# Kernel optimization log

Hardware: AMD Instinct MI355X
Metric: run time of the kernel (lower is better)

Reference implementation:

```python
import jax, jax.numpy as jnp
import numpy as np

T, B, H, D = 128, 8, 8, 64


def setup_inputs() -> dict:
    key = jax.random.key(0)
    kA, kB, kS = jax.random.split(key, 3)
    # Gated-delta transition matrices: near-identity contractions so the
    # length-T matrix-product recurrence is numerically stable, mimicking
    # A_t = gamma_t * (I - beta_t k_t k_t^T) of the gated delta rule.
    eye = jnp.eye(D, dtype=jnp.float32)
    A = 0.9 * eye + 0.06 * jax.random.normal(kA, (T, B, H, D, D), dtype=jnp.float32)
    Bm = jax.random.normal(kB, (T, B, H, D, D), dtype=jnp.float32)
    init_state = jax.random.normal(kS, (B, H, D, D), dtype=jnp.float32)
    return {"A": A, "Bm": Bm, "init_state": init_state}


def reference(A, Bm, init_state):
    """Gated delta rule recurrence S_t = S_{t-1} @ A_t + B_t for all t,
    computed with a parallel associative scan (Blelloch-equivalent).

    A:  [T,B,H,D,D] transition matrices
    Bm: [T,B,H,D,D] additive updates
    init_state: [B,H,D,D]
    returns states: [T,B,H,D,D]
    """
    def combine(e1, e2):
        # apply e1 first, then e2:
        # (S A1 + B1) A2 + B2 = S (A1 A2) + (B1 A2 + B2)
        A1, B1 = e1
        A2, B2 = e2
        A12 = jnp.einsum('tbhij,tbhjk->tbhik', A1, A2)
        B12 = jnp.einsum('tbhij,tbhjk->tbhik', B1, A2) + B2
        return (A12, B12)

    cumA, cumB = jax.lax.associative_scan(combine, (A, Bm), axis=0)
    # S_t = init_state @ cumA_t + cumB_t
    states = jnp.einsum('bhij,tbhjk->tbhik', init_state, cumA) + cumB
    return states
```

## Files before the change

### kernel.cpp

```cpp
#include <hip/hip_runtime.h>


constexpr int kT = 128;
constexpr int kBH = 64;
constexpr int kD = 64;
constexpr int kNC = 8;
constexpr int kCH = kT / kNC;
constexpr int kP = 68;
constexpr int kTile = kD * kD;

typedef __attribute__((ext_vector_type(8))) short short8;
typedef __attribute__((ext_vector_type(4))) short short4v;
typedef __attribute__((ext_vector_type(4))) float f32x4;

__device__ __forceinline__ unsigned short f2bf(float f) {
  unsigned int u = __float_as_uint(f);
  u += 0x7FFFu + ((u >> 16) & 1u);
  return (unsigned short)(u >> 16);
}
__device__ __forceinline__ float bf2f(unsigned short h) {
  return __uint_as_float(((unsigned int)h) << 16);
}
__device__ __forceinline__ int swzi(int r, int c) { return (r * 64 + c) ^ ((r & 7) << 3); }

__device__ __forceinline__ const float* tile_ptr(const float* base, int t, int bh) {
  return base + ((size_t)(t * kBH + bh)) * kTile;
}

__device__ __forceinline__ f32x4 mfma16(short8 a, short8 b, f32x4 c) {
  return __builtin_amdgcn_mfma_f32_16x16x32_bf16(a, b, c, 0, 0, 0);
}

__device__ __forceinline__ void split4(const f32x4 v, short4v& h, short4v& l) {
#pragma unroll
  for (int i = 0; i < 4; ++i) {
    const unsigned short hh = f2bf(v[i]);
    h[i] = (short)hh;
    l[i] = (short)f2bf(v[i] - bf2f(hh));
  }
}

__global__ __launch_bounds__(256, 2) void gdr_k1(
    const float* __restrict__ A, const float* __restrict__ Bm,
    float* __restrict__ PA, float* __restrict__ PB) {
  __shared__ unsigned short sAh[4096], sAl[4096];
  __shared__ unsigned short sPAh[4096], sPAl[4096];
  __shared__ unsigned short sPBh[4096], sPBl[4096];

  const int tid = threadIdx.x;
  const int lane = tid & 63, wave = tid >> 6;
  const int wr = wave >> 1, wc = wave & 1;
  const int q = lane >> 4, l15 = lane & 15;
  const int bh = blockIdx.x >> 3, ck = blockIdx.x & 7;
  const int t0 = ck * kCH;
  const int an = lane;
  const int akb = wave;

  f32x4 apa[2][2], apb[2][2];
  {
    const float* At = tile_ptr(A, t0, bh);
    const float* Bt = tile_ptr(Bm, t0, bh);
#pragma unroll
    for (int mi = 0; mi < 2; ++mi)
#pragma unroll
      for (int ni = 0; ni < 2; ++ni) {
        const int off = (wc * 32 + ni * 16 + l15) * 64 + wr * 32 + mi * 16 + q * 4;
        apa[mi][ni] = *reinterpret_cast<const f32x4*>(At + off);
        apb[mi][ni] = *reinterpret_cast<const f32x4*>(Bt + off);
      }
  }

  float pfA[16];
  f32x4 pfB[2][2];
  {
    const float* At = tile_ptr(A, t0 + 1, bh);
    const float* Bt = tile_ptr(Bm, t0 + 1, bh);
#pragma unroll
    for (int kk = 0; kk < 16; ++kk) pfA[kk] = At[(akb * 16 + kk) * 64 + an];
#pragma unroll
    for (int mi = 0; mi < 2; ++mi)
#pragma unroll
      for (int ni = 0; ni < 2; ++ni)
        pfB[mi][ni] = *reinterpret_cast<const f32x4*>(
            Bt + (wc * 32 + ni * 16 + l15) * 64 + wr * 32 + mi * 16 + q * 4);
  }

  for (int t = t0 + 1; t < t0 + kCH; ++t) {
    if (t > t0 + 1) __syncthreads();
#pragma unroll
    for (int mi = 0; mi < 2; ++mi)
#pragma unroll
      for (int ni = 0; ni < 2; ++ni) {
        const int b = wc * 32 + ni * 16 + l15;
        const int a0 = wr * 32 + mi * 16 + q * 4;
        const int idx = swzi(b, a0);
        short4v h, l;
        split4(apa[mi][ni], h, l);
        *reinterpret_cast<short4v*>(&sPAh[idx]) = h;
        *reinterpret_cast<short4v*>(&sPAl[idx]) = l;
        split4(apb[mi][ni], h, l);
        *reinterpret_cast<short4v*>(&sPBh[idx]) = h;
        *reinterpret_cast<short4v*>(&sPBl[idx]) = l;
      }
#pragma unroll
    for (int s = 0; s < 2; ++s) {
      short8 h, l;
#pragma unroll
      for (int j = 0; j < 8; ++j) {
        const float v = pfA[s * 8 + j];
        const unsigned short hh = f2bf(v);
        h[j] = (short)hh;
        l[j] = (short)f2bf(v - bf2f(hh));
      }
      const int idx = swzi(an, akb * 16 + s * 8);
      *reinterpret_cast<short8*>(&sAh[idx]) = h;
      *reinterpret_cast<short8*>(&sAl[idx]) = l;
    }
    __syncthreads();

#pragma unroll
    for (int mi = 0; mi < 2; ++mi)
#pragma unroll
      for (int ni = 0; ni < 2; ++ni) {
        apa[mi][ni] = (f32x4){0.f, 0.f, 0.f, 0.f};
        apb[mi][ni] = pfB[mi][ni];
      }

    const int tn = (t + 1 < t0 + kCH) ? t + 1 : t;
    {
      const float* At = tile_ptr(A, tn, bh);
      const float* Bt = tile_ptr(Bm, tn, bh);
#pragma unroll
      for (int kk = 0; kk < 16; ++kk) pfA[kk] = At[(akb * 16 + kk) * 64 + an];
#pragma unroll
      for (int mi = 0; mi < 2; ++mi)
#pragma unroll
        for (int ni = 0; ni < 2; ++ni)
          pfB[mi][ni] = *reinterpret_cast<const f32x4*>(
              Bt + (wc * 32 + ni * 16 + l15) * 64 + wr * 32 + mi * 16 + q * 4);
    }

#pragma unroll
    for (int ks = 0; ks < 2; ++ks) {
      short8 xh[2], xl[2], yah[2], yal[2], ybh[2], ybl[2];
      const int colb = ks * 32 + q * 8;
#pragma unroll
      for (int mi = 0; mi < 2; ++mi) {
        const int idx = swzi(wr * 32 + mi * 16 + l15, colb);
        xh[mi] = *reinterpret_cast<const short8*>(&sAh[idx]);
        xl[mi] = *reinterpret_cast<const short8*>(&sAl[idx]);
      }
#pragma unroll
      for (int ni = 0; ni < 2; ++ni) {
        const int idx = swzi(wc * 32 + ni * 16 + l15, colb);
        yah[ni] = *reinterpret_cast<const short8*>(&sPAh[idx]);
        yal[ni] = *reinterpret_cast<const short8*>(&sPAl[idx]);
        ybh[ni] = *reinterpret_cast<const short8*>(&sPBh[idx]);
        ybl[ni] = *reinterpret_cast<const short8*>(&sPBl[idx]);
      }
#pragma unroll
      for (int mi = 0; mi < 2; ++mi)
#pragma unroll
        for (int ni = 0; ni < 2; ++ni) {
          apa[mi][ni] = mfma16(xh[mi], yah[ni], apa[mi][ni]);
          apa[mi][ni] = mfma16(xh[mi], yal[ni], apa[mi][ni]);
          apa[mi][ni] = mfma16(xl[mi], yah[ni], apa[mi][ni]);
          apb[mi][ni] = mfma16(xh[mi], ybh[ni], apb[mi][ni]);
          apb[mi][ni] = mfma16(xh[mi], ybl[ni], apb[mi][ni]);
          apb[mi][ni] = mfma16(xl[mi], ybh[ni], apb[mi][ni]);
        }
    }
  }

  float* pao = PA + (size_t)blockIdx.x * kTile;
  float* pbo = PB + (size_t)blockIdx.x * kTile;
#pragma unroll
  for (int mi = 0; mi < 2; ++mi)
#pragma unroll
    for (int ni = 0; ni < 2; ++ni) {
      const int off = (wc * 32 + ni * 16 + l15) * 64 + wr * 32 + mi * 16 + q * 4;
      *reinterpret_cast<f32x4*>(pao + off) = apa[mi][ni];
      *reinterpret_cast<f32x4*>(pbo + off) = apb[mi][ni];
    }
}

__global__ __launch_bounds__(256, 2) void gdr_k2(
    const float* __restrict__ PA, const float* __restrict__ PB,
    const float* __restrict__ S0, float* __restrict__ Sst) {
  __shared__ float sST[kD * kP];
  __shared__ float sPA[kD * kP];
  const int tid = threadIdx.x;
  const int bh = blockIdx.x;
  const int ti = tid >> 4, tj = tid & 15;
  const int r0 = ti << 2, c0 = tj << 2;
  const int sr = tid >> 2, sc = (tid & 3) << 4;

  float s[4][4];
  {
    const float* Sb = S0 + (size_t)bh * kTile;
#pragma unroll
    for (int ii = 0; ii < 4; ++ii) {
      const float4 v = *reinterpret_cast<const float4*>(Sb + (r0 + ii) * kD + c0);
      s[ii][0] = v.x; s[ii][1] = v.y; s[ii][2] = v.z; s[ii][3] = v.w;
    }
  }
  {
    float* o = Sst + (size_t)(bh * kNC) * kTile;
#pragma unroll
    for (int ii = 0; ii < 4; ++ii)
      *reinterpret_cast<float4*>(o + (r0 + ii) * kD + c0) =
          make_float4(s[ii][0], s[ii][1], s[ii][2], s[ii][3]);
  }

  for (int ck = 0; ck < kNC - 1; ++ck) {
    if (ck) __syncthreads();
#pragma unroll
    for (int jj = 0; jj < 4; ++jj)
      *reinterpret_cast<float4*>(&sST[(c0 + jj) * kP + r0]) =
          make_float4(s[0][jj], s[1][jj], s[2][jj], s[3][jj]);
    {
      const float* Pt = PA + (size_t)(bh * kNC + ck) * kTile;
#pragma unroll
      for (int w = 0; w < 4; ++w)
        *reinterpret_cast<float4*>(&sPA[sr * kP + sc + 4 * w]) =
            *reinterpret_cast<const float4*>(Pt + sr * kD + sc + 4 * w);
    }
    __syncthreads();
    {
      const float* Qt = PB + (size_t)(bh * kNC + ck) * kTile;
#pragma unroll
      for (int ii = 0; ii < 4; ++ii) {
        const float4 v = *reinterpret_cast<const float4*>(Qt + (r0 + ii) * kD + c0);
        s[ii][0] = v.x; s[ii][1] = v.y; s[ii][2] = v.z; s[ii][3] = v.w;
      }
    }
#pragma unroll 4
    for (int k = 0; k < kD; ++k) {
      const float4 va = *reinterpret_cast<const float4*>(&sPA[k * kP + c0]);
      const float4 ss = *reinterpret_cast<const float4*>(&sST[k * kP + r0]);
      const float af[4] = {va.x, va.y, va.z, va.w};
      const float sf[4] = {ss.x, ss.y, ss.z, ss.w};
#pragma unroll
      for (int ii = 0; ii < 4; ++ii)
#pragma unroll
        for (int jj = 0; jj < 4; ++jj)
          s[ii][jj] += sf[ii] * af[jj];
    }
    {
      float* o = Sst + (size_t)(bh * kNC + ck + 1) * kTile;
#pragma unroll
      for (int ii = 0; ii < 4; ++ii)
        *reinterpret_cast<float4*>(o + (r0 + ii) * kD + c0) =
            make_float4(s[ii][0], s[ii][1], s[ii][2], s[ii][3]);
    }
  }
}

__global__ __launch_bounds__(256, 2) void gdr_k3(
    const float* __restrict__ A, const float* __restrict__ Bm,
    const float* __restrict__ Sst, float* __restrict__ out) {
  __shared__ unsigned short sAh[4096], sAl[4096];
  __shared__ unsigned short sSh[4096], sSl[4096];

  const int tid = threadIdx.x;
  const int lane = tid & 63, wave = tid >> 6;
  const int wr = wave >> 1, wc = wave & 1;
  const int q = lane >> 4, l15 = lane & 15;
  const int bh = blockIdx.x >> 3, ck = blockIdx.x & 7;
  const int t0 = ck * kCH;
  const int an = lane;
  const int akb = wave;

  f32x4 acc[2][2];
  {
    const float* Sb = Sst + (size_t)blockIdx.x * kTile;
#pragma unroll
    for (int mi = 0; mi < 2; ++mi)
#pragma unroll
      for (int ni = 0; ni < 2; ++ni)
        acc[mi][ni] = *reinterpret_cast<const f32x4*>(
            Sb + (wc * 32 + ni * 16 + l15) * 64 + wr * 32 + mi * 16 + q * 4);
  }

  float pfA[16];
  f32x4 pfB[2][2];
  {
    const float* At = tile_ptr(A, t0, bh);
    const float* Bt = tile_ptr(Bm, t0, bh);
#pragma unroll
    for (int kk = 0; kk < 16; ++kk) pfA[kk] = At[(akb * 16 + kk) * 64 + an];
#pragma unroll
    for (int mi = 0; mi < 2; ++mi)
#pragma unroll
      for (int ni = 0; ni < 2; ++ni)
        pfB[mi][ni] = *reinterpret_cast<const f32x4*>(
            Bt + (wc * 32 + ni * 16 + l15) * 64 + wr * 32 + mi * 16 + q * 4);
  }

  for (int t = t0; t < t0 + kCH; ++t) {
    if (t > t0) __syncthreads();
#pragma unroll
    for (int mi = 0; mi < 2; ++mi)
#pragma unroll
      for (int ni = 0; ni < 2; ++ni) {
        const int b = wc * 32 + ni * 16 + l15;
        const int a0 = wr * 32 + mi * 16 + q * 4;
        const int idx = swzi(b, a0);
        short4v h, l;
        split4(acc[mi][ni], h, l);
        *reinterpret_cast<short4v*>(&sSh[idx]) = h;
        *reinterpret_cast<short4v*>(&sSl[idx]) = l;
      }
#pragma unroll
    for (int s = 0; s < 2; ++s) {
      short8 h, l;
#pragma unroll
      for (int j = 0; j < 8; ++j) {
        const float v = pfA[s * 8 + j];
        const unsigned short hh = f2bf(v);
        h[j] = (short)hh;
        l[j] = (short)f2bf(v - bf2f(hh));
      }
      const int idx = swzi(an, akb * 16 + s * 8);
      *reinterpret_cast<short8*>(&sAh[idx]) = h;
      *reinterpret_cast<short8*>(&sAl[idx]) = l;
    }
    __syncthreads();

#pragma unroll
    for (int mi = 0; mi < 2; ++mi)
#pragma unroll
      for (int ni = 0; ni < 2; ++ni)
        acc[mi][ni] = pfB[mi][ni];

    const int tn = (t + 1 < t0 + kCH) ? t + 1 : t;
    {
      const float* At = tile_ptr(A, tn, bh);
      const float* Bt = tile_ptr(Bm, tn, bh);
#pragma unroll
      for (int kk = 0; kk < 16; ++kk) pfA[kk] = At[(akb * 16 + kk) * 64 + an];
#pragma unroll
      for (int mi = 0; mi < 2; ++mi)
#pragma unroll
        for (int ni = 0; ni < 2; ++ni)
          pfB[mi][ni] = *reinterpret_cast<const f32x4*>(
              Bt + (wc * 32 + ni * 16 + l15) * 64 + wr * 32 + mi * 16 + q * 4);
    }

#pragma unroll
    for (int ks = 0; ks < 2; ++ks) {
      short8 xh[2], xl[2], yh[2], yl[2];
      const int colb = ks * 32 + q * 8;
#pragma unroll
      for (int mi = 0; mi < 2; ++mi) {
        const int idx = swzi(wr * 32 + mi * 16 + l15, colb);
        xh[mi] = *reinterpret_cast<const short8*>(&sAh[idx]);
        xl[mi] = *reinterpret_cast<const short8*>(&sAl[idx]);
      }
#pragma unroll
      for (int ni = 0; ni < 2; ++ni) {
        const int idx = swzi(wc * 32 + ni * 16 + l15, colb);
        yh[ni] = *reinterpret_cast<const short8*>(&sSh[idx]);
        yl[ni] = *reinterpret_cast<const short8*>(&sSl[idx]);
      }
#pragma unroll
      for (int mi = 0; mi < 2; ++mi)
#pragma unroll
        for (int ni = 0; ni < 2; ++ni) {
          acc[mi][ni] = mfma16(xh[mi], yh[ni], acc[mi][ni]);
          acc[mi][ni] = mfma16(xh[mi], yl[ni], acc[mi][ni]);
          acc[mi][ni] = mfma16(xl[mi], yh[ni], acc[mi][ni]);
        }
    }

    float* o = out + ((size_t)(t * kBH + bh)) * kTile;
#pragma unroll
    for (int mi = 0; mi < 2; ++mi)
#pragma unroll
      for (int ni = 0; ni < 2; ++ni) {
        const int off = (wc * 32 + ni * 16 + l15) * 64 + wr * 32 + mi * 16 + q * 4;
        *reinterpret_cast<f32x4*>(o + off) = acc[mi][ni];
      }
  }
}

extern "C" void kernel_launch(void* const* d_in, const int* in_sizes, int n_in,
                              void* d_out, int out_size, void* d_ws, size_t ws_size,
                              hipStream_t stream) {
  const float* A  = (const float*)d_in[0];
  const float* Bm = (const float*)d_in[1];
  const float* S0 = (const float*)d_in[2];
  float* out = (float*)d_out;

  float* PA  = (float*)d_ws;
  float* PB  = PA + (size_t)kBH * kNC * kTile;
  float* Sst = PB + (size_t)kBH * kNC * kTile;

  gdr_k1<<<dim3(kBH * kNC), dim3(256), 0, stream>>>(A, Bm, PA, PB);
  gdr_k2<<<dim3(kBH), dim3(256), 0, stream>>>(PA, PB, S0, Sst);
  gdr_k3<<<dim3(kBH * kNC), dim3(256), 0, stream>>>(A, Bm, Sst, out);
}
```

Measured before the change: 161.1 us.

## Replace three-stage chunked scan with hierarchical five-pass scan and more chunks

Generalizes the chunk-fold and chunk-scan kernels with stride parameters so they can be reused at two levels. Chunks are folded, then groups of four chunk products are folded again, then a short serial scan runs over groups, a scan over chunk boundaries within groups, and a final per-step scan that writes all states. The number of chunks rises to 16 or 32 when the workspace is large enough, shortening each block's serial chain and raising the block count. The cost is more kernel launches, more workspace traffic, and more intermediate products that are rounded through split-bf16 MFMA.

Result: slower. 184.7 us (+14.6%).

```diff
diff --git a/kernel.cpp b/kernel.cpp
--- a/kernel.cpp
+++ b/kernel.cpp
@@ -4,9 +4,6 @@
 constexpr int kT = 128;
 constexpr int kBH = 64;
 constexpr int kD = 64;
-constexpr int kNC = 8;
-constexpr int kCH = kT / kNC;
-constexpr int kP = 68;
 constexpr int kTile = kD * kD;
 
 typedef __attribute__((ext_vector_type(8))) short short8;
@@ -23,10 +20,6 @@
 }
 __device__ __forceinline__ int swzi(int r, int c) { return (r * 64 + c) ^ ((r & 7) << 3); }
 
-__device__ __forceinline__ const float* tile_ptr(const float* base, int t, int bh) {
-  return base + ((size_t)(t * kBH + bh)) * kTile;
-}
-
 __device__ __forceinline__ f32x4 mfma16(short8 a, short8 b, f32x4 c) {
   return __builtin_amdgcn_mfma_f32_16x16x32_bf16(a, b, c, 0, 0, 0);
 }
@@ -40,9 +33,10 @@
   }
 }
 
-__global__ __launch_bounds__(256, 2) void gdr_k1(
-    const float* __restrict__ A, const float* __restrict__ Bm,
-    float* __restrict__ PA, float* __restrict__ PB) {
+__global__ __launch_bounds__(256, 2) void gdr_fold(
+    const float* __restrict__ srcA, const float* __restrict__ srcB,
+    float* __restrict__ dstA, float* __restrict__ dstB,
+    int perChain, long chainBase, long idxBase, long elemStride, int nElem) {
   __shared__ unsigned short sAh[4096], sAl[4096];
   __shared__ unsigned short sPAh[4096], sPAl[4096];
   __shared__ unsigned short sPBh[4096], sPBl[4096];
@@ -51,15 +45,14 @@
   const int lane = tid & 63, wave = tid >> 6;
   const int wr = wave >> 1, wc = wave & 1;
   const int q = lane >> 4, l15 = lane & 15;
-  const int bh = blockIdx.x >> 3, ck = blockIdx.x & 7;
-  const int t0 = ck * kCH;
-  const int an = lane;
-  const int akb = wave;
+  const int bh = blockIdx.x / perChain, id = blockIdx.x % perChain;
+  const long e0 = (long)bh * chainBase + (long)id * idxBase;
+  const int an = lane, akb = wave;
 
   f32x4 apa[2][2], apb[2][2];
   {
-    const float* At = tile_ptr(A, t0, bh);
-    const float* Bt = tile_ptr(Bm, t0, bh);
+    const float* At = srcA + (size_t)e0 * kTile;
+    const float* Bt = srcB + (size_t)e0 * kTile;
 #pragma unroll
     for (int mi = 0; mi < 2; ++mi)
 #pragma unroll
@@ -73,8 +66,8 @@
   float pfA[16];
   f32x4 pfB[2][2];
   {
-    const float* At = tile_ptr(A, t0 + 1, bh);
-    const float* Bt = tile_ptr(Bm, t0 + 1, bh);
+    const float* At = srcA + (size_t)(e0 + elemStride) * kTile;
+    const float* Bt = srcB + (size_t)(e0 + elemStride) * kTile;
 #pragma unroll
     for (int kk = 0; kk < 16; ++kk) pfA[kk] = At[(akb * 16 + kk) * 64 + an];
 #pragma unroll
@@ -85,8 +78,8 @@
             Bt + (wc * 32 + ni * 16 + l15) * 64 + wr * 32 + mi * 16 + q * 4);
   }
 
-  for (int t = t0 + 1; t < t0 + kCH; ++t) {
-    if (t > t0 + 1) __syncthreads();
+  for (int i = 1; i < nElem; ++i) {
+    if (i > 1) __syncthreads();
 #pragma unroll
     for (int mi = 0; mi < 2; ++mi)
 #pragma unroll
@@ -126,10 +119,10 @@
         apb[mi][ni] = pfB[mi][ni];
       }
 
-    const int tn = (t + 1 < t0 + kCH) ? t + 1 : t;
+    const int in = (i + 1 < nElem) ? i + 1 : i;
     {
-      const float* At = tile_ptr(A, tn, bh);
-      const float* Bt = tile_ptr(Bm, tn, bh);
+      const float* At = srcA + (size_t)(e0 + (long)in * elemStride) * kTile;
+      const float* Bt = srcB + (size_t)(e0 + (long)in * elemStride) * kTile;
 #pragma unroll
       for (int kk = 0; kk < 16; ++kk) pfA[kk] = At[(akb * 16 + kk) * 64 + an];
 #pragma unroll
@@ -172,8 +165,8 @@
     }
   }
 
-  float* pao = PA + (size_t)blockIdx.x * kTile;
-  float* pbo = PB + (size_t)blockIdx.x * kTile;
+  float* pao = dstA + (size_t)blockIdx.x * kTile;
+  float* pbo = dstB + (size_t)blockIdx.x * kTile;
 #pragma unroll
   for (int mi = 0; mi < 2; ++mi)
 #pragma unroll
@@ -184,81 +177,11 @@
     }
 }
 
-__global__ __launch_bounds__(256, 2) void gdr_k2(
-    const float* __restrict__ PA, const float* __restrict__ PB,
-    const float* __restrict__ S0, float* __restrict__ Sst) {
-  __shared__ float sST[kD * kP];
-  __shared__ float sPA[kD * kP];
-  const int tid = threadIdx.x;
-  const int bh = blockIdx.x;
-  const int ti = tid >> 4, tj = tid & 15;
-  const int r0 = ti << 2, c0 = tj << 2;
-  const int sr = tid >> 2, sc = (tid & 3) << 4;
-
-  float s[4][4];
-  {
-    const float* Sb = S0 + (size_t)bh * kTile;
-#pragma unroll
-    for (int ii = 0; ii < 4; ++ii) {
-      const float4 v = *reinterpret_cast<const float4*>(Sb + (r0 + ii) * kD + c0);
-      s[ii][0] = v.x; s[ii][1] = v.y; s[ii][2] = v.z; s[ii][3] = v.w;
-    }
-  }
-  {
-    float* o = Sst + (size_t)(bh * kNC) * kTile;
-#pragma unroll
-    for (int ii = 0; ii < 4; ++ii)
-      *reinterpret_cast<float4*>(o + (r0 + ii) * kD + c0) =
-          make_float4(s[ii][0], s[ii][1], s[ii][2], s[ii][3]);
-  }
-
-  for (int ck = 0; ck < kNC - 1; ++ck) {
-    if (ck) __syncthreads();
-#pragma unroll
-    for (int jj = 0; jj < 4; ++jj)
-      *reinterpret_cast<float4*>(&sST[(c0 + jj) * kP + r0]) =
-          make_float4(s[0][jj], s[1][jj], s[2][jj], s[3][jj]);
-    {
-      const float* Pt = PA + (size_t)(bh * kNC + ck) * kTile;
-#pragma unroll
-      for (int w = 0; w < 4; ++w)
-        *reinterpret_cast<float4*>(&sPA[sr * kP + sc + 4 * w]) =
-            *reinterpret_cast<const float4*>(Pt + sr * kD + sc + 4 * w);
-    }
-    __syncthreads();
-    {
-      const float* Qt = PB + (size_t)(bh * kNC + ck) * kTile;
-#pragma unroll
-      for (int ii = 0; ii < 4; ++ii) {
-        const float4 v = *reinterpret_cast<const float4*>(Qt + (r0 + ii) * kD + c0);
-        s[ii][0] = v.x; s[ii][1] = v.y; s[ii][2] = v.z; s[ii][3] = v.w;
-      }
-    }
-#pragma unroll 4
-    for (int k = 0; k < kD; ++k) {
-      const float4 va = *reinterpret_cast<const float4*>(&sPA[k * kP + c0]);
-      const float4 ss = *reinterpret_cast<const float4*>(&sST[k * kP + r0]);
-      const float af[4] = {va.x, va.y, va.z, va.w};
-      const float sf[4] = {ss.x, ss.y, ss.z, ss.w};
-#pragma unroll
-      for (int ii = 0; ii < 4; ++ii)
-#pragma unroll
-        for (int jj = 0; jj < 4; ++jj)
-          s[ii][jj] += sf[ii] * af[jj];
-    }
-    {
-      float* o = Sst + (size_t)(bh * kNC + ck + 1) * kTile;
-#pragma unroll
-      for (int ii = 0; ii < 4; ++ii)
-        *reinterpret_cast<float4*>(o + (r0 + ii) * kD + c0) =
-            make_float4(s[ii][0], s[ii][1], s[ii][2], s[ii][3]);
-    }
-  }
-}
-
-__global__ __launch_bounds__(256, 2) void gdr_k3(
-    const float* __restrict__ A, const float* __restrict__ Bm,
-    const float* __restrict__ Sst, float* __restrict__ out) {
+__global__ __launch_bounds__(256, 2) void gdr_scan(
+    const float* __restrict__ srcA, const float* __restrict__ srcB,
+    const float* __restrict__ S0, float* __restrict__ out,
+    int perChain, long chainBase, long idxBase, long elemStride,
+    int nSteps, int tbMul, int tStep) {
   __shared__ unsigned short sAh[4096], sAl[4096];
   __shared__ unsigned short sSh[4096], sSl[4096];
 
@@ -266,14 +189,15 @@
   const int lane = tid & 63, wave = tid >> 6;
   const int wr = wave >> 1, wc = wave & 1;
   const int q = lane >> 4, l15 = lane & 15;
-  const int bh = blockIdx.x >> 3, ck = blockIdx.x & 7;
-  const int t0 = ck * kCH;
-  const int an = lane;
-  const int akb = wave;
+  const int bh = blockIdx.x / perChain, id = blockIdx.x % perChain;
+  const long e0 = (long)bh * chainBase + (long)id * idxBase;
+  const int tBase = id * tbMul;
+  const int an = lane, akb = wave;
 
   f32x4 acc[2][2];
   {
-    const float* Sb = Sst + (size_t)blockIdx.x * kTile;
+    const float* Sb = (tBase == 0) ? (S0 + (size_t)bh * kTile)
+                                   : (out + ((size_t)(tBase - 1) * kBH + bh) * kTile);
 #pragma unroll
     for (int mi = 0; mi < 2; ++mi)
 #pragma unroll
@@ -285,8 +209,8 @@
   float pfA[16];
   f32x4 pfB[2][2];
   {
-    const float* At = tile_ptr(A, t0, bh);
-    const float* Bt = tile_ptr(Bm, t0, bh);
+    const float* At = srcA + (size_t)e0 * kTile;
+    const float* Bt = srcB + (size_t)e0 * kTile;
 #pragma unroll
     for (int kk = 0; kk < 16; ++kk) pfA[kk] = At[(akb * 16 + kk) * 64 + an];
 #pragma unroll
@@ -297,8 +221,8 @@
             Bt + (wc * 32 + ni * 16 + l15) * 64 + wr * 32 + mi * 16 + q * 4);
   }
 
-  for (int t = t0; t < t0 + kCH; ++t) {
-    if (t > t0) __syncthreads();
+  for (int i = 0; i < nSteps; ++i) {
+    if (i) __syncthreads();
 #pragma unroll
     for (int mi = 0; mi < 2; ++mi)
 #pragma unroll
@@ -333,10 +257,10 @@
       for (int ni = 0; ni < 2; ++ni)
         acc[mi][ni] = pfB[mi][ni];
 
-    const int tn = (t + 1 < t0 + kCH) ? t + 1 : t;
+    const int in = (i + 1 < nSteps) ? i + 1 : i;
     {
-      const float* At = tile_ptr(A, tn, bh);
-      const float* Bt = tile_ptr(Bm, tn, bh);
+      const float* At = srcA + (size_t)(e0 + (long)in * elemStride) * kTile;
+      const float* Bt = srcB + (size_t)(e0 + (long)in * elemStride) * kTile;
 #pragma unroll
       for (int kk = 0; kk < 16; ++kk) pfA[kk] = At[(akb * 16 + kk) * 64 + an];
 #pragma unroll
@@ -373,7 +297,8 @@
         }
     }
 
-    float* o = out + ((size_t)(t * kBH + bh)) * kTile;
+    const int t = tBase + (i + 1) * tStep - 1;
+    float* o = out + ((size_t)t * kBH + bh) * kTile;
 #pragma unroll
     for (int mi = 0; mi < 2; ++mi)
 #pragma unroll
@@ -392,11 +317,26 @@
   const float* S0 = (const float*)d_in[2];
   float* out = (float*)d_out;
 
-  float* PA  = (float*)d_ws;
-  float* PB  = PA + (size_t)kBH * kNC * kTile;
-  float* Sst = PB + (size_t)kBH * kNC * kTile;
-
-  gdr_k1<<<dim3(kBH * kNC), dim3(256), 0, stream>>>(A, Bm, PA, PB);
-  gdr_k2<<<dim3(kBH), dim3(256), 0, stream>>>(PA, PB, S0, Sst);
-  gdr_k3<<<dim3(kBH * kNC), dim3(256), 0, stream>>>(A, Bm, Sst, out);
-}
+  int NC;
+  if (ws_size >= (size_t)5120 * kTile * 4)      NC = 32;
+  else if (ws_size >= (size_t)2560 * kTile * 4) NC = 16;
+  else                                          NC = 8;
+  const int CH = kT / NC;
+  const int NG = NC / 4;
+
+  float* PA = (float*)d_ws;
+  float* PB = PA + (size_t)kBH * NC * kTile;
+  float* GA = PB + (size_t)kBH * NC * kTile;
+  float* GB = GA + (size_t)kBH * NG * kTile;
+
+  gdr_fold<<<dim3(kBH * NC), dim3(256), 0, stream>>>(
+      A, Bm, PA, PB, NC, 1L, (long)CH * kBH, (long)kBH, CH);
+  gdr_fold<<<dim3(kBH * NG), dim3(256), 0, stream>>>(
+      PA, PB, GA, GB, NG, (long)NC, 4L, 1L, 4);
+  gdr_scan<<<dim3(kBH), dim3(256), 0, stream>>>(
+      GA, GB, S0, out, 1, (long)NG, 0L, 1L, NG, 0, 4 * CH);
+  gdr_scan<<<dim3(kBH * NG), dim3(256), 0, stream>>>(
+      PA, PB, S0, out, NG, (long)NC, 4L, 1L, 3, 4 * CH, CH);
+  gdr_scan<<<dim3(kBH * NC), dim3(256), 0, stream>>>(
+      A, Bm, S0, out, NC, 1L, (long)CH * kBH, (long)kBH, CH - 1, CH, 1);
+}
```
